# Performance work log

Measured on AMD Instinct MI355X. Metric: run time of the kernel, lower is better.

## Reference

```python
import jax, jax.numpy as jnp
import numpy as np

D_MODEL = 1024
N_HEAD = 16
D_K = D_MODEL // N_HEAD
D_FF = 2048
EPS = 1e-6
SCALE = np.sqrt(D_K).astype(np.float32)


def layer_norm(x, alpha, beta):
    # Faithful to source: unbiased std (ddof=1), eps added to std
    mean = jnp.mean(x, axis=-1, keepdims=True)
    std = jnp.std(x, axis=-1, keepdims=True, ddof=1) + EPS
    return alpha * (x - mean) / std + beta


def setup_inputs() -> dict:
    key = jax.random.key(0)
    ks = jax.random.split(key, 12)
    s = 0.02
    return {
        "x": jax.random.normal(ks[0], (4, 1024, D_MODEL), dtype=jnp.float32),
        "Wq": jax.random.normal(ks[1], (D_MODEL, D_MODEL), dtype=jnp.float32) * s,
        "bq": jax.random.normal(ks[2], (D_MODEL,), dtype=jnp.float32) * s,
        "Wo": jax.random.normal(ks[3], (D_MODEL, D_MODEL), dtype=jnp.float32) * s,
        "bo": jax.random.normal(ks[4], (D_MODEL,), dtype=jnp.float32) * s,
        "W1": jax.random.normal(ks[5], (D_MODEL, D_FF), dtype=jnp.float32) * s,
        "b1": jax.random.normal(ks[6], (D_FF,), dtype=jnp.float32) * s,
        "W2": jax.random.normal(ks[7], (D_FF, D_MODEL), dtype=jnp.float32) * s,
        "b2": jax.random.normal(ks[8], (D_MODEL,), dtype=jnp.float32) * s,
        "alpha": jnp.ones((D_MODEL,), dtype=jnp.float32),
        "beta": jnp.ones((D_MODEL,), dtype=jnp.float32),
    }


def reference(x, Wq, bq, Wo, bo, W1, b1, W2, b2, alpha, beta):
    b, s, d = x.shape
    # Source bug kept: q, k, v all use q_linear
    def proj(t):
        return (t @ Wq + bq).reshape(b, s, N_HEAD, D_K).transpose(0, 2, 1, 3)
    q = proj(x)  # [b,h,s,dk]
    k = proj(x)
    v = proj(x)
    scores = jnp.einsum('bhqd,bhkd->bhqk', q, k) / SCALE
    scores = jax.nn.softmax(scores, axis=-1)
    z = jnp.einsum('bhqk,bhkd->bhqd', scores, v)
    concat = z.transpose(0, 2, 1, 3).reshape(b, s, d)
    attn_out = concat @ Wo + bo
    x = layer_norm(x + attn_out, alpha, beta)
    ff = jax.nn.relu(x @ W1 + b1) @ W2 + b2
    x = layer_norm(x + ff, alpha, beta)  # source reuses norm_1
    return x
```

## Files before the change

kernel.cpp:

```cpp
#include <hip/hip_runtime.h>
#include <hip/hip_bf16.h>
#include <stdint.h>

#define TOK   4096
#define DMODEL 1024
#define DFF    2048
#define NHEAD  16
#define DK     64

typedef unsigned short u16;
typedef __attribute__((ext_vector_type(8))) short short8;
typedef __attribute__((ext_vector_type(4))) float f32x4;

typedef __attribute__((address_space(1))) void gvoid;
typedef __attribute__((address_space(3))) void lvoid;

#define QSCALE   0.35355339f
#define QUNSCALE 2.82842712f

__device__ __forceinline__ u16 f2b(float f) {
    uint32_t x = __builtin_bit_cast(uint32_t, f);
    x += 0x7FFFu + ((x >> 16) & 1u);
    return (u16)(x >> 16);
}
__device__ __forceinline__ float b2f(u16 u) {
    uint32_t x = ((uint32_t)u) << 16;
    return __builtin_bit_cast(float, x);
}
__device__ __forceinline__ uint32_t f2b2(float lo, float hi) {
    return (uint32_t)f2b(lo) | ((uint32_t)f2b(hi) << 16);
}
__device__ __forceinline__ uint32_t cvtpk(float lo, float hi) {
    uint32_t r;
    asm("v_cvt_pk_bf16_f32 %0, %1, %2" : "=v"(r) : "v"(lo), "v"(hi));
    return r;
}

__device__ __forceinline__ void gload16(const void* g, void* l) {
    __builtin_amdgcn_global_load_lds((gvoid*)g, (lvoid*)l, 16, 0, 0);
}

__device__ __forceinline__ void cvt_tr_dev(
    const float* __restrict__ W, u16* __restrict__ Wt, int K, int N,
    int bx, int by, int tid, u16 (*T)[68])
{
    const int tx = tid & 15, ty = tid >> 4;
    const int n0 = bx * 64, k0 = by * 64;
#pragma unroll
    for (int i = 0; i < 4; i++) {
        int k = ty + i * 16;
        float4 v = *(const float4*)&W[(size_t)(k0 + k) * N + n0 + tx * 4];
        T[tx * 4 + 0][k] = f2b(v.x);
        T[tx * 4 + 1][k] = f2b(v.y);
        T[tx * 4 + 2][k] = f2b(v.z);
        T[tx * 4 + 3][k] = f2b(v.w);
    }
    __syncthreads();
#pragma unroll
    for (int i = 0; i < 4; i++) {
        int n = ty + i * 16;
        ushort4 o;
        o.x = T[n][tx * 4 + 0]; o.y = T[n][tx * 4 + 1];
        o.z = T[n][tx * 4 + 2]; o.w = T[n][tx * 4 + 3];
        *(ushort4*)&Wt[(size_t)(n0 + n) * K + k0 + tx * 4] = o;
    }
}

__global__ __launch_bounds__(256) void prep1(
    const float* __restrict__ Wq, u16* __restrict__ Wqt,
    const float* __restrict__ x, u16* __restrict__ xb)
{
    __shared__ u16 T[64][68];
    const int id = blockIdx.x, tid = threadIdx.x;
    if (id < 256) {
        cvt_tr_dev(Wq, Wqt, 1024, 1024, id & 15, id >> 4, tid, T);
    } else {
        size_t base = (size_t)(id - 256) * 1024 + tid;
#pragma unroll
        for (int j = 0; j < 4; j++) {
            float4 v = ((const float4*)x)[base + j * 256];
            ((uint2*)xb)[base + j * 256] =
                make_uint2(f2b2(v.x, v.y), f2b2(v.z, v.w));
        }
    }
}

template<int BM, int BN, bool RELU, bool OUTBF16, bool QOUT>
__global__ __launch_bounds__(256) void gemm_mfma(
    const u16* __restrict__ A, const u16* __restrict__ Bt,
    const float* __restrict__ bias, void* __restrict__ Cv,
    u16* __restrict__ CT, float oscale,
    int M, int N, int K)
{
    constexpr int MF = BM / 32;
    constexpr int NF = BN / 32;
    constexpr int ASTR = BM * 64;
    constexpr int BSTR = BN * 64;
    __shared__ __align__(16) u16 As[2 * ASTR];
    __shared__ __align__(16) u16 Bs[2 * BSTR];

    const int tid  = threadIdx.x;
    const int lane = tid & 63;
    const int wid  = tid >> 6;
    const int wm = wid >> 1, wn = wid & 1;
    const int frow = lane & 15, fk = lane >> 4;

    const int gx = N / BN;
    const int gy = M / BM;
    const int rpx = gy >> 3;
    const int L = blockIdx.x;
    const int xcd = L & 7, within = L >> 3;
    const int yy = xcd * rpx + within / gx;
    const int xx = within % gx;

    const int row0 = yy * BM;
    const int col0 = xx * BN;

    const u16* gA[MF]; u16* lA[MF];
    const u16* gB[NF]; u16* lB[NF];
#pragma unroll
    for (int inst = 0; inst < MF; inst++) {
        int s = inst * 256 + tid;
        int r = s >> 3;
        int kc = ((s & 7) ^ (r & 7)) * 8;
        gA[inst] = A + (size_t)(row0 + r) * K + kc;
        lA[inst] = As + inst * 2048 + wid * 512;
    }
#pragma unroll
    for (int inst = 0; inst < NF; inst++) {
        int s = inst * 256 + tid;
        int r = s >> 3;
        int kc = ((s & 7) ^ (r & 7)) * 8;
        gB[inst] = Bt + (size_t)(col0 + r) * K + kc;
        lB[inst] = Bs + inst * 2048 + wid * 512;
    }

    int aoff[MF][2], boff[NF][2];
#pragma unroll
    for (int m = 0; m < MF; m++) {
        int r = wm * (BM / 2) + m * 16 + frow;
#pragma unroll
        for (int kk = 0; kk < 2; kk++)
            aoff[m][kk] = r * 64 + (((kk << 2) + fk) ^ (r & 7)) * 8;
    }
#pragma unroll
    for (int n = 0; n < NF; n++) {
        int r = wn * (BN / 2) + n * 16 + frow;
#pragma unroll
        for (int kk = 0; kk < 2; kk++)
            boff[n][kk] = r * 64 + (((kk << 2) + fk) ^ (r & 7)) * 8;
    }

    f32x4 acc[MF][NF] = {};
    const int nT = K >> 6;

#pragma unroll
    for (int inst = 0; inst < MF; inst++) gload16(gA[inst], lA[inst]);
#pragma unroll
    for (int inst = 0; inst < NF; inst++) gload16(gB[inst], lB[inst]);
    __syncthreads();

    for (int t = 0; t < nT; t++) {
        const int cur = t & 1;
        if (t + 1 < nT) {
            const int k0 = (t + 1) << 6;
#pragma unroll
            for (int inst = 0; inst < MF; inst++)
                gload16(gA[inst] + k0, lA[inst] + (cur ^ 1) * ASTR);
#pragma unroll
            for (int inst = 0; inst < NF; inst++)
                gload16(gB[inst] + k0, lB[inst] + (cur ^ 1) * BSTR);
        }

        const u16* Ab = As + cur * ASTR;
        const u16* Bb = Bs + cur * BSTR;
        short8 a[MF][2], b[NF][2];
#pragma unroll
        for (int m = 0; m < MF; m++)
#pragma unroll
            for (int kk = 0; kk < 2; kk++)
                a[m][kk] = *(const short8*)(Ab + aoff[m][kk]);
#pragma unroll
        for (int n = 0; n < NF; n++)
#pragma unroll
            for (int kk = 0; kk < 2; kk++)
                b[n][kk] = *(const short8*)(Bb + boff[n][kk]);

#pragma unroll
        for (int m = 0; m < MF; m++)
#pragma unroll
            for (int n = 0; n < NF; n++)
#pragma unroll
                for (int kk = 0; kk < 2; kk++)
                    acc[m][n] = __builtin_amdgcn_mfma_f32_16x16x32_bf16(
                        a[m][kk], b[n][kk], acc[m][n], 0, 0, 0);

        __syncthreads();
    }

#pragma unroll
    for (int n = 0; n < NF; n++) {
        const int gcol = col0 + wn * (BN / 2) + n * 16 + frow;
        const float bv = bias[gcol];
#pragma unroll
        for (int m = 0; m < MF; m++) {
            const int grow0 = row0 + wm * (BM / 2) + m * 16 + fk * 4;
            float v[4];
#pragma unroll
            for (int i = 0; i < 4; i++) {
                v[i] = (acc[m][n][i] + bv) * oscale;
                if (RELU) v[i] = fmaxf(v[i], 0.0f);
                if (OUTBF16)
                    ((u16*)Cv)[(size_t)(grow0 + i) * N + gcol] = f2b(v[i]);
                else
                    ((float*)Cv)[(size_t)(grow0 + i) * N + gcol] = v[i];
            }
            if (QOUT) {
                const int hh = gcol >> 6, d = gcol & 63;
                const int bb = grow0 >> 10, sl = grow0 & 1023;
                *(uint2*)&CT[(((size_t)(bb * 16 + hh) * 64 + d) << 10) + sl] =
                    make_uint2(f2b2(v[0], v[1]), f2b2(v[2], v[3]));
            }
        }
    }
}

__global__ __launch_bounds__(256, 2) void attn_prepw(
    const u16* __restrict__ qb, const u16* __restrict__ qT,
    u16* __restrict__ zb,
    const float* __restrict__ Wo, const float* __restrict__ W1,
    const float* __restrict__ W2,
    u16* __restrict__ Wot, u16* __restrict__ W1t, u16* __restrict__ W2t)
{
    __shared__ __align__(16) u16 Ks[2][64 * 64];
    __shared__ __align__(16) u16 Kt[2][64 * 64];
    __shared__ __align__(16) u16 Ps[128 * 64];

    const int tid = threadIdx.x;
    const int id  = blockIdx.x;

    if (id >= 512) {
        u16 (*T)[68] = reinterpret_cast<u16 (*)[68]>(&Ks[0][0]);
        int t = id - 512;
        if (t < 256)       cvt_tr_dev(Wo, Wot, 1024, 1024, t & 15, t >> 4, tid, T);
        else if (t < 768)  { t -= 256; cvt_tr_dev(W1, W1t, 1024, 2048, t & 31, t >> 5, tid, T); }
        else               { t -= 768; cvt_tr_dev(W2, W2t, 2048, 1024, t & 15, t >> 4, tid, T); }
        return;
    }

    const int lane = tid & 63;
    const int w    = tid >> 6;
    const int frow = lane & 15, fk = lane >> 4;

    const int h  = id & 15;
    const int qt = (id >> 4) & 7;
    const int b  = id >> 7;
    const int q0 = qt * 128;

    const u16* qhead = qb + ((size_t)b * 1024) * 1024 + h * 64;
    const u16* thead = qT + ((size_t)(b * 16 + h) * 64) * 1024;

#pragma unroll
    for (int inst = 0; inst < 2; inst++) {
        int s = inst * 256 + tid, r = s >> 3, kc = ((s & 7) ^ (r & 7)) * 8;
        gload16(qhead + (size_t)r * 1024 + kc, Ks[0] + inst * 2048 + w * 512);
        gload16(thead + (size_t)r * 1024 + kc, Kt[0] + inst * 2048 + w * 512);
    }

    short8 qf[2][2];
#pragma unroll
    for (int m = 0; m < 2; m++) {
        int r = q0 + w * 32 + m * 16 + frow;
#pragma unroll
        for (int kk = 0; kk < 2; kk++)
            qf[m][kk] = *(const short8*)(qhead + (size_t)r * 1024 + kk * 32 + fk * 8);
    }

    float lp[2] = {};
    f32x4 o[2][4] = {};

    __syncthreads();

    for (int t = 0; t < 16; t++) {
        const int cur = t & 1;
        if (t < 15) {
            const int kv = (t + 1) * 64;
#pragma unroll
            for (int inst = 0; inst < 2; inst++) {
                int s = inst * 256 + tid, r = s >> 3, kc = ((s & 7) ^ (r & 7)) * 8;
                gload16(qhead + (size_t)(kv + r) * 1024 + kc,
                        Ks[cur ^ 1] + inst * 2048 + w * 512);
                gload16(thead + (size_t)r * 1024 + kv + kc,
                        Kt[cur ^ 1] + inst * 2048 + w * 512);
            }
        }

        short8 kf[4][2];
#pragma unroll
        for (int n = 0; n < 4; n++) {
            int r = n * 16 + frow;
#pragma unroll
            for (int kk = 0; kk < 2; kk++)
                kf[n][kk] = *(const short8*)(Ks[cur] + r * 64 +
                                             (((kk << 2) + fk) ^ (r & 7)) * 8);
        }
        f32x4 st[4][2] = {};
        __builtin_amdgcn_s_setprio(1);
#pragma unroll
        for (int nk = 0; nk < 4; nk++)
#pragma unroll
            for (int mq = 0; mq < 2; mq++)
#pragma unroll
                for (int kk = 0; kk < 2; kk++)
                    st[nk][mq] = __builtin_amdgcn_mfma_f32_16x16x32_bf16(
                        kf[nk][kk], qf[mq][kk], st[nk][mq], 0, 0, 0);
        __builtin_amdgcn_s_setprio(0);

#pragma unroll
        for (int mq = 0; mq < 2; mq++) {
            const int r = w * 32 + mq * 16 + frow;
            const int rb = r * 64, sw = (r & 7) << 3;
#pragma unroll
            for (int nk = 0; nk < 4; nk++) {
                float p0 = __expf(st[nk][mq][0]);
                float p1 = __expf(st[nk][mq][1]);
                float p2 = __expf(st[nk][mq][2]);
                float p3 = __expf(st[nk][mq][3]);
                lp[mq] += (p0 + p1) + (p2 + p3);
                *(uint2*)&Ps[rb + ((nk * 16 + fk * 4) ^ sw)] =
                    make_uint2(cvtpk(p0, p1), cvtpk(p2, p3));
            }
        }

        short8 pa[2][2], vf[4][2];
#pragma unroll
        for (int m = 0; m < 2; m++) {
            int r = w * 32 + m * 16 + frow;
#pragma unroll
            for (int kk = 0; kk < 2; kk++)
                pa[m][kk] = *(const short8*)(Ps + r * 64 +
                                             (((kk << 2) + fk) ^ (r & 7)) * 8);
        }
#pragma unroll
        for (int n = 0; n < 4; n++) {
            int r = n * 16 + frow;
#pragma unroll
            for (int kk = 0; kk < 2; kk++)
                vf[n][kk] = *(const short8*)(Kt[cur] + r * 64 +
                                             (((kk << 2) + fk) ^ (r & 7)) * 8);
        }
        __builtin_amdgcn_s_setprio(1);
#pragma unroll
        for (int m = 0; m < 2; m++)
#pragma unroll
            for (int n = 0; n < 4; n++)
#pragma unroll
                for (int kk = 0; kk < 2; kk++)
                    o[m][n] = __builtin_amdgcn_mfma_f32_16x16x32_bf16(
                        pa[m][kk], vf[n][kk], o[m][n], 0, 0, 0);
        __builtin_amdgcn_s_setprio(0);

        __syncthreads();
    }

#pragma unroll
    for (int mq = 0; mq < 2; mq++) {
        lp[mq] += __shfl_xor(lp[mq], 16);
        lp[mq] += __shfl_xor(lp[mq], 32);
    }
#pragma unroll
    for (int m = 0; m < 2; m++)
#pragma unroll
        for (int i = 0; i < 4; i++) {
            const float lfull = __shfl(lp[m], fk * 4 + i);
            const float rl = QUNSCALE / lfull;
            const size_t gr = (size_t)(b * 1024 + q0 + w * 32 + m * 16 + fk * 4 + i);
#pragma unroll
            for (int n = 0; n < 4; n++)
                zb[gr * 1024 + h * 64 + n * 16 + frow] = f2b(o[m][n][i] * rl);
        }
}

__device__ __forceinline__ float4 ld4(const float* p) { return *(const float4*)p; }
__device__ __forceinline__ float4 ld4(const u16* p) {
    ushort4 u = *(const ushort4*)p;
    return make_float4(b2f(u.x), b2f(u.y), b2f(u.z), b2f(u.w));
}
__device__ __forceinline__ void st4(float* p, float4 v) { *(float4*)p = v; }
__device__ __forceinline__ void st4(u16* p, float4 v) {
    *(uint2*)p = make_uint2(f2b2(v.x, v.y), f2b2(v.z, v.w));
}

template<typename TA, typename TB, typename TO>
__global__ __launch_bounds__(256) void add_ln(
    const TA* __restrict__ a, const TB* __restrict__ b,
    const float* __restrict__ alpha, const float* __restrict__ beta,
    TO* __restrict__ out)
{
    const int row = blockIdx.x;
    const int c = threadIdx.x * 4;
    float4 va = ld4(a + (size_t)row * DMODEL + c);
    float4 vb = ld4(b + (size_t)row * DMODEL + c);
    float v0 = va.x + vb.x, v1 = va.y + vb.y;
    float v2 = va.z + vb.z, v3 = va.w + vb.w;

    float sum = (v0 + v1) + (v2 + v3);
    float sq  = (v0 * v0 + v1 * v1) + (v2 * v2 + v3 * v3);
#pragma unroll
    for (int off = 32; off > 0; off >>= 1) {
        sum += __shfl_xor(sum, off);
        sq  += __shfl_xor(sq, off);
    }
    __shared__ float s1[4], s2[4];
    const int wid = threadIdx.x >> 6, lane = threadIdx.x & 63;
    if (lane == 0) { s1[wid] = sum; s2[wid] = sq; }
    __syncthreads();
    sum = (s1[0] + s1[1]) + (s1[2] + s1[3]);
    sq  = (s2[0] + s2[1]) + (s2[2] + s2[3]);

    const float mean = sum * (1.0f / 1024.0f);
    float var = (sq - 1024.0f * mean * mean) * (1.0f / 1023.0f);
    var = fmaxf(var, 0.0f);
    const float rdenom = 1.0f / (sqrtf(var) + 1e-6f);

    float4 al = *(const float4*)(alpha + c);
    float4 be = *(const float4*)(beta + c);
    float4 r;
    r.x = al.x * (v0 - mean) * rdenom + be.x;
    r.y = al.y * (v1 - mean) * rdenom + be.y;
    r.z = al.z * (v2 - mean) * rdenom + be.z;
    r.w = al.w * (v3 - mean) * rdenom + be.w;
    st4(out + (size_t)row * DMODEL + c, r);
}

extern "C" void kernel_launch(void* const* d_in, const int* in_sizes, int n_in,
                              void* d_out, int out_size, void* d_ws, size_t ws_size,
                              hipStream_t stream) {
    const float* x     = (const float*)d_in[0];
    const float* Wq    = (const float*)d_in[1];
    const float* bq    = (const float*)d_in[2];
    const float* Wo    = (const float*)d_in[3];
    const float* bo    = (const float*)d_in[4];
    const float* W1    = (const float*)d_in[5];
    const float* b1    = (const float*)d_in[6];
    const float* W2    = (const float*)d_in[7];
    const float* b2    = (const float*)d_in[8];
    const float* alpha = (const float*)d_in[9];
    const float* beta  = (const float*)d_in[10];

    char* base = (char*)d_ws;
    u16* Wqt = (u16*)base;
    u16* Wot = (u16*)(base + (2u  << 20));
    u16* W1t = (u16*)(base + (4u  << 20));
    u16* W2t = (u16*)(base + (8u  << 20));
    u16* zb  = (u16*)(base + (12u << 20));
    u16* x1b = zb;
    u16* qb  = (u16*)(base + (20u << 20));
    u16* g2  = qb;
    u16* qT  = (u16*)(base + (28u << 20));
    u16* g   = qT;
    u16* xb  = (u16*)(base + (36u << 20));
    u16* hb  = (u16*)(base + (36u << 20));

    dim3 blk(256);

    prep1<<<dim3(1280), blk, 0, stream>>>(Wq, Wqt, x, xb);

    gemm_mfma<128, 64, false, true, true><<<dim3(512), blk, 0, stream>>>(
        xb, Wqt, bq, qb, qT, QSCALE, TOK, 1024, 1024);
    attn_prepw<<<dim3(1792), blk, 0, stream>>>(
        qb, qT, zb, Wo, W1, W2, Wot, W1t, W2t);
    gemm_mfma<128, 64, false, true, false><<<dim3(512), blk, 0, stream>>>(
        zb, Wot, bo, g, nullptr, 1.0f, TOK, 1024, 1024);
    add_ln<u16, u16, u16><<<dim3(TOK), blk, 0, stream>>>(xb, g, alpha, beta, x1b);
    gemm_mfma<128, 128, true, true, false><<<dim3(512), blk, 0, stream>>>(
        x1b, W1t, b1, hb, nullptr, 1.0f, TOK, 2048, 1024);
    gemm_mfma<128, 64, false, true, false><<<dim3(512), blk, 0, stream>>>(
        hb, W2t, b2, g2, nullptr, 1.0f, TOK, 1024, 2048);
    add_ln<u16, u16, float><<<dim3(TOK), blk, 0, stream>>>(
        x1b, g2, alpha, beta, (float*)d_out);
}
```

Baseline: 141.3 us.

## Replace 4-wave GEMM with single-wave 64x64 tiles and barrier-free prefetch

```diff
diff --git a/kernel.cpp b/kernel.cpp
--- a/kernel.cpp
+++ b/kernel.cpp
@@ -85,126 +85,115 @@
     }
 }
 
-template<int BM, int BN, bool RELU, bool OUTBF16, bool QOUT>
-__global__ __launch_bounds__(256) void gemm_mfma(
+template<bool RELU, bool OUTBF16, bool QOUT>
+__global__ __launch_bounds__(64) void gemm_w(
     const u16* __restrict__ A, const u16* __restrict__ Bt,
     const float* __restrict__ bias, void* __restrict__ Cv,
     u16* __restrict__ CT, float oscale,
     int M, int N, int K)
 {
-    constexpr int MF = BM / 32;
-    constexpr int NF = BN / 32;
-    constexpr int ASTR = BM * 64;
-    constexpr int BSTR = BN * 64;
-    __shared__ __align__(16) u16 As[2 * ASTR];
-    __shared__ __align__(16) u16 Bs[2 * BSTR];
-
-    const int tid  = threadIdx.x;
-    const int lane = tid & 63;
-    const int wid  = tid >> 6;
-    const int wm = wid >> 1, wn = wid & 1;
+    __shared__ __align__(16) u16 As[2 * 4096];
+    __shared__ __align__(16) u16 Bs[2 * 4096];
+
+    const int lane = threadIdx.x;
     const int frow = lane & 15, fk = lane >> 4;
 
-    const int gx = N / BN;
-    const int gy = M / BM;
+    const int gx = N >> 6;
+    const int gy = M >> 6;
     const int rpx = gy >> 3;
     const int L = blockIdx.x;
     const int xcd = L & 7, within = L >> 3;
     const int yy = xcd * rpx + within / gx;
     const int xx = within % gx;
 
-    const int row0 = yy * BM;
-    const int col0 = xx * BN;
-
-    const u16* gA[MF]; u16* lA[MF];
-    const u16* gB[NF]; u16* lB[NF];
-#pragma unroll
-    for (int inst = 0; inst < MF; inst++) {
-        int s = inst * 256 + tid;
+    const int row0 = yy * 64;
+    const int col0 = xx * 64;
+
+    const u16* gA[8]; const u16* gB[8];
+#pragma unroll
+    for (int inst = 0; inst < 8; inst++) {
+        int s = inst * 64 + lane;
         int r = s >> 3;
         int kc = ((s & 7) ^ (r & 7)) * 8;
-        gA[inst] = A + (size_t)(row0 + r) * K + kc;
-        lA[inst] = As + inst * 2048 + wid * 512;
-    }
-#pragma unroll
-    for (int inst = 0; inst < NF; inst++) {
-        int s = inst * 256 + tid;
-        int r = s >> 3;
-        int kc = ((s & 7) ^ (r & 7)) * 8;
+        gA[inst] = A  + (size_t)(row0 + r) * K + kc;
         gB[inst] = Bt + (size_t)(col0 + r) * K + kc;
-        lB[inst] = Bs + inst * 2048 + wid * 512;
-    }
-
-    int aoff[MF][2], boff[NF][2];
-#pragma unroll
-    for (int m = 0; m < MF; m++) {
-        int r = wm * (BM / 2) + m * 16 + frow;
-#pragma unroll
-        for (int kk = 0; kk < 2; kk++)
+    }
+
+    int aoff[4][2], boff[4][2];
+#pragma unroll
+    for (int m = 0; m < 4; m++) {
+        int r = m * 16 + frow;
+#pragma unroll
+        for (int kk = 0; kk < 2; kk++) {
             aoff[m][kk] = r * 64 + (((kk << 2) + fk) ^ (r & 7)) * 8;
-    }
-#pragma unroll
-    for (int n = 0; n < NF; n++) {
-        int r = wn * (BN / 2) + n * 16 + frow;
-#pragma unroll
-        for (int kk = 0; kk < 2; kk++)
-            boff[n][kk] = r * 64 + (((kk << 2) + fk) ^ (r & 7)) * 8;
-    }
-
-    f32x4 acc[MF][NF] = {};
+            boff[m][kk] = aoff[m][kk];
+        }
+    }
+
+    f32x4 acc[4][4] = {};
     const int nT = K >> 6;
 
 #pragma unroll
-    for (int inst = 0; inst < MF; inst++) gload16(gA[inst], lA[inst]);
-#pragma unroll
-    for (int inst = 0; inst < NF; inst++) gload16(gB[inst], lB[inst]);
-    __syncthreads();
+    for (int inst = 0; inst < 8; inst++) {
+        gload16(gA[inst], As + inst * 512);
+        gload16(gB[inst], Bs + inst * 512);
+    }
+#pragma unroll
+    for (int inst = 0; inst < 8; inst++) {
+        gload16(gA[inst] + 64, As + 4096 + inst * 512);
+        gload16(gB[inst] + 64, Bs + 4096 + inst * 512);
+    }
+    asm volatile("s_waitcnt vmcnt(16)" ::: "memory");
+    __builtin_amdgcn_sched_barrier(0);
 
     for (int t = 0; t < nT; t++) {
         const int cur = t & 1;
-        if (t + 1 < nT) {
-            const int k0 = (t + 1) << 6;
-#pragma unroll
-            for (int inst = 0; inst < MF; inst++)
-                gload16(gA[inst] + k0, lA[inst] + (cur ^ 1) * ASTR);
-#pragma unroll
-            for (int inst = 0; inst < NF; inst++)
-                gload16(gB[inst] + k0, lB[inst] + (cur ^ 1) * BSTR);
-        }
-
-        const u16* Ab = As + cur * ASTR;
-        const u16* Bb = Bs + cur * BSTR;
-        short8 a[MF][2], b[NF][2];
-#pragma unroll
-        for (int m = 0; m < MF; m++)
-#pragma unroll
-            for (int kk = 0; kk < 2; kk++)
+        const u16* Ab = As + cur * 4096;
+        const u16* Bb = Bs + cur * 4096;
+
+        short8 a[4][2], b[4][2];
+#pragma unroll
+        for (int m = 0; m < 4; m++)
+#pragma unroll
+            for (int kk = 0; kk < 2; kk++) {
                 a[m][kk] = *(const short8*)(Ab + aoff[m][kk]);
-#pragma unroll
-        for (int n = 0; n < NF; n++)
-#pragma unroll
-            for (int kk = 0; kk < 2; kk++)
-                b[n][kk] = *(const short8*)(Bb + boff[n][kk]);
-
-#pragma unroll
-        for (int m = 0; m < MF; m++)
-#pragma unroll
-            for (int n = 0; n < NF; n++)
+                b[m][kk] = *(const short8*)(Bb + boff[m][kk]);
+            }
+
+        asm volatile("s_waitcnt lgkmcnt(0)" ::: "memory");
+        __builtin_amdgcn_sched_barrier(0);
+        if (t + 2 < nT) {
+            const int k0 = (t + 2) << 6;
+#pragma unroll
+            for (int inst = 0; inst < 8; inst++) {
+                gload16(gA[inst] + k0, As + cur * 4096 + inst * 512);
+                gload16(gB[inst] + k0, Bs + cur * 4096 + inst * 512);
+            }
+        }
+
+#pragma unroll
+        for (int m = 0; m < 4; m++)
+#pragma unroll
+            for (int n = 0; n < 4; n++)
 #pragma unroll
                 for (int kk = 0; kk < 2; kk++)
                     acc[m][n] = __builtin_amdgcn_mfma_f32_16x16x32_bf16(
                         a[m][kk], b[n][kk], acc[m][n], 0, 0, 0);
 
-        __syncthreads();
-    }
-
-#pragma unroll
-    for (int n = 0; n < NF; n++) {
-        const int gcol = col0 + wn * (BN / 2) + n * 16 + frow;
+        if (t + 1 < nT) {
+            if (t + 2 < nT) asm volatile("s_waitcnt vmcnt(16)" ::: "memory");
+            else            asm volatile("s_waitcnt vmcnt(0)"  ::: "memory");
+            __builtin_amdgcn_sched_barrier(0);
+        }
+    }
+
+#pragma unroll
+    for (int n = 0; n < 4; n++) {
+        const int gcol = col0 + n * 16 + frow;
         const float bv = bias[gcol];
 #pragma unroll
-        for (int m = 0; m < MF; m++) {
-            const int grow0 = row0 + wm * (BM / 2) + m * 16 + fk * 4;
+        for (int m = 0; m < 4; m++) {
+            const int grow0 = row0 + m * 16 + fk * 4;
             float v[4];
 #pragma unroll
             for (int i = 0; i < 4; i++) {
@@ -463,19 +452,20 @@
     u16* hb  = (u16*)(base + (36u << 20));
 
     dim3 blk(256);
+    dim3 wblk(64);
 
     prep1<<<dim3(1280), blk, 0, stream>>>(Wq, Wqt, x, xb);
 
-    gemm_mfma<128, 64, false, true, true><<<dim3(512), blk, 0, stream>>>(
+    gemm_w<false, true, true><<<dim3(1024), wblk, 0, stream>>>(
         xb, Wqt, bq, qb, qT, QSCALE, TOK, 1024, 1024);
     attn_prepw<<<dim3(1792), blk, 0, stream>>>(
         qb, qT, zb, Wo, W1, W2, Wot, W1t, W2t);
-    gemm_mfma<128, 64, false, true, false><<<dim3(512), blk, 0, stream>>>(
+    gemm_w<false, true, false><<<dim3(1024), wblk, 0, stream>>>(
         zb, Wot, bo, g, nullptr, 1.0f, TOK, 1024, 1024);
     add_ln<u16, u16, u16><<<dim3(TOK), blk, 0, stream>>>(xb, g, alpha, beta, x1b);
-    gemm_mfma<128, 128, true, true, false><<<dim3(512), blk, 0, stream>>>(
+    gemm_w<true, true, false><<<dim3(2048), wblk, 0, stream>>>(
         x1b, W1t, b1, hb, nullptr, 1.0f, TOK, 2048, 1024);
-    gemm_mfma<128, 64, false, true, false><<<dim3(512), blk, 0, stream>>>(
+    gemm_w<false, true, false><<<dim3(1024), wblk, 0, stream>>>(
         hb, W2t, b2, g2, nullptr, 1.0f, TOK, 1024, 2048);
     add_ln<u16, u16, float><<<dim3(TOK), blk, 0, stream>>>(
         x1b, g2, alpha, beta, (float*)d_out);
```

Measured after the change: 137.9 us. 1.02x faster.
